# Kernel optimization log

Hardware: AMD Instinct MI355X
Metric: run time of the kernel (lower is better)

The kernel has to match this reference:

```python
import jax, jax.numpy as jnp
import numpy as np

NEG_SLOPE = 0.2


def _gat_conv(x, src, dst, W, a_l, a_r, b, n_nodes, activate):
    """DGL-style GATConv. x:[N,F_in], W:[F_in,H*D], a_l/a_r/b:[H,D]."""
    H, D = a_l.shape
    feat = (x @ W).reshape(n_nodes, H, D)                      # [N,H,D]
    el = jnp.sum(feat * a_l, axis=-1)                          # [N,H]
    er = jnp.sum(feat * a_r, axis=-1)                          # [N,H]
    e = jax.nn.leaky_relu(el[src] + er[dst], NEG_SLOPE)        # [E,H]
    # edge softmax over incoming edges of each dst node (numerically stable)
    emax = jax.ops.segment_max(e, dst, num_segments=n_nodes)   # [N,H]
    emax = jnp.where(jnp.isfinite(emax), emax, 0.0)            # zero-in-degree safe
    ee = jnp.exp(e - emax[dst])                                # [E,H]
    denom = jax.ops.segment_sum(ee, dst, num_segments=n_nodes) # [N,H]
    alpha = ee / jnp.maximum(denom[dst], 1e-9)                 # [E,H]
    # aggregate alpha-weighted src features into dst
    msg = alpha[:, :, None] * feat[src]                        # [E,H,D]
    out = jax.ops.segment_sum(msg, dst, num_segments=n_nodes)  # [N,H,D]
    out = out + b
    if activate:
        out = jax.nn.elu(out)
    return out


def setup_inputs() -> dict:
    key = jax.random.key(0)
    ks = jax.random.split(key, 16)
    N, E, F_in, H, Dh, C = 50000, 800000, 256, 4, 64, 40
    s = lambda fan_in: 1.0 / np.sqrt(fan_in)
    return {
        "x": jax.random.normal(ks[0], (N, F_in), dtype=jnp.float32),
        "edge_index": jax.random.randint(ks[1], (2, E), 0, N, dtype=jnp.int32),
        "W0": jax.random.normal(ks[2], (F_in, H * Dh), dtype=jnp.float32) * s(F_in),
        "al0": jax.random.normal(ks[3], (H, Dh), dtype=jnp.float32) * s(Dh),
        "ar0": jax.random.normal(ks[4], (H, Dh), dtype=jnp.float32) * s(Dh),
        "b0": jnp.zeros((H, Dh), dtype=jnp.float32),
        "W1": jax.random.normal(ks[5], (H * Dh, H * Dh), dtype=jnp.float32) * s(H * Dh),
        "al1": jax.random.normal(ks[6], (H, Dh), dtype=jnp.float32) * s(Dh),
        "ar1": jax.random.normal(ks[7], (H, Dh), dtype=jnp.float32) * s(Dh),
        "b1": jnp.zeros((H, Dh), dtype=jnp.float32),
        "W2": jax.random.normal(ks[8], (H * Dh, H * C), dtype=jnp.float32) * s(H * Dh),
        "al2": jax.random.normal(ks[9], (H, C), dtype=jnp.float32) * s(C),
        "ar2": jax.random.normal(ks[10], (H, C), dtype=jnp.float32) * s(C),
        "b2": jnp.zeros((H, C), dtype=jnp.float32),
    }


def reference(x, edge_index, W0, al0, ar0, b0, W1, al1, ar1, b1, W2, al2, ar2, b2):
    N = x.shape[0]
    src, dst = edge_index[0], edge_index[1]
    h = _gat_conv(x, src, dst, W0, al0, ar0, b0, N, activate=True).reshape(N, -1)
    h = _gat_conv(h, src, dst, W1, al1, ar1, b1, N, activate=True).reshape(N, -1)
    out = _gat_conv(h, src, dst, W2, al2, ar2, b2, N, activate=False)
    logits = out.mean(axis=1)  # mean over heads -> [N, num_classes]
    return logits
```

## Files before the change

kernel.cpp:

```cpp
#include <hip/hip_runtime.h>
#include <hip/hip_bf16.h>
#include <math.h>

#define NEG_SLOPE 0.2f

typedef unsigned short ushortT;
typedef __attribute__((ext_vector_type(8))) short short8;
typedef __attribute__((ext_vector_type(4))) float f32x4;

static __device__ __forceinline__ float leaky(float x){ return x > 0.f ? x : NEG_SLOPE * x; }
static __device__ __forceinline__ float elu(float x){ return x > 0.f ? x : (__expf(x) - 1.f); }

static __device__ __forceinline__ ushortT f2bf(float f){
  unsigned u = __float_as_uint(f);
  u += 0x7fff + ((u >> 16) & 1);
  return (ushortT)(u >> 16);
}
static __device__ __forceinline__ float bf2f(ushortT h){ return __uint_as_float((unsigned)h << 16); }
static __device__ __forceinline__ float bf_lo(unsigned u){ return __uint_as_float(u << 16); }
static __device__ __forceinline__ float bf_hi(unsigned u){ return __uint_as_float(u & 0xffff0000u); }


__global__ void hist_kernel(const int* __restrict__ dst, int E, int* __restrict__ counts){
  int i = blockIdx.x*blockDim.x + threadIdx.x;
  if(i < E) atomicAdd(&counts[dst[i]], 1);
}

__global__ void scan1_kernel(const int* __restrict__ counts, int N,
                             int* __restrict__ offsets, int* __restrict__ blocksums){
  __shared__ int sdata[1024];
  int i = blockIdx.x*1024 + threadIdx.x;
  int v = (i<N) ? counts[i] : 0;
  sdata[threadIdx.x] = v;
  __syncthreads();
  for(int off=1; off<1024; off<<=1){
    int t = (threadIdx.x >= off) ? sdata[threadIdx.x-off] : 0;
    __syncthreads();
    sdata[threadIdx.x] += t;
    __syncthreads();
  }
  if(i<N) offsets[i] = sdata[threadIdx.x] - v;
  if(threadIdx.x==1023) blocksums[blockIdx.x] = sdata[1023];
}

__global__ void scan2_kernel(int* __restrict__ blocksums, int nb){
  __shared__ int sdata[64];
  int v = ((int)threadIdx.x < nb) ? blocksums[threadIdx.x] : 0;
  sdata[threadIdx.x] = v;
  __syncthreads();
  for(int off=1; off<64; off<<=1){
    int t = (threadIdx.x >= off) ? sdata[threadIdx.x-off] : 0;
    __syncthreads();
    sdata[threadIdx.x] += t;
    __syncthreads();
  }
  if((int)threadIdx.x < nb) blocksums[threadIdx.x] = sdata[threadIdx.x] - v;
}

__global__ void scan3_kernel(int* __restrict__ offsets, const int* __restrict__ blocksums,
                             int N, int E, int* __restrict__ cursor){
  int i = blockIdx.x*1024 + threadIdx.x;
  if(i < N){
    int o = offsets[i] + blocksums[blockIdx.x];
    offsets[i] = o;
    cursor[i] = o;
  }
  if(i == 0) offsets[N] = E;
}

__global__ void scatter_kernel(const int* __restrict__ src, const int* __restrict__ dst, int E,
                               int* __restrict__ cursor, int* __restrict__ ssrc,
                               int* __restrict__ sdst){
  int i = blockIdx.x*blockDim.x + threadIdx.x;
  if(i < E){
    int d = dst[i];
    int p = atomicAdd(&cursor[d], 1);
    ssrc[p] = src[i];
    sdst[p] = d;
  }
}

__global__ __launch_bounds__(256) void wsplit_pack(const float* __restrict__ W, int N,
                              ushortT* __restrict__ Wh, ushortT* __restrict__ Wl){
  int idx = blockIdx.x*256 + threadIdx.x;
  int lane = idx & 63;
  int t  = (idx >> 6) & 7;
  int nt = idx >> 9;
  int l15 = lane & 15, quad = lane >> 4;
  int n = nt*16 + l15;
  ushortT h[8], l[8];
  #pragma unroll
  for(int j=0;j<8;j++){
    int k = t*32 + quad*8 + j;
    float v = (n < N) ? W[(size_t)k*N + n] : 0.f;
    h[j] = f2bf(v);
    l[j] = f2bf(v - bf2f(h[j]));
  }
  *(short8*)&Wh[(size_t)idx*8] = *(short8*)h;
  *(short8*)&Wl[(size_t)idx*8] = *(short8*)l;
}

__global__ __launch_bounds__(256) void xsplit_pack(const float* __restrict__ x, int M, int Mpad,
                              ushortT* __restrict__ Xh, ushortT* __restrict__ Xl){
  int idx = blockIdx.x*256 + threadIdx.x;
  if(idx >= 8*Mpad) return;
  int t = idx / Mpad, m = idx - t*Mpad;
  size_t base = (size_t)idx * 32;
  if(m < M){
    const float* xr = &x[(size_t)m*256 + t*32];
    #pragma unroll
    for(int c=0;c<4;c++){
      float4 v0 = *(const float4*)&xr[c*8];
      float4 v1 = *(const float4*)&xr[c*8+4];
      float vv[8] = {v0.x,v0.y,v0.z,v0.w,v1.x,v1.y,v1.z,v1.w};
      ushortT h[8], l[8];
      #pragma unroll
      for(int j=0;j<8;j++){
        h[j] = f2bf(vv[j]);
        l[j] = f2bf(vv[j] - bf2f(h[j]));
      }
      *(short8*)&Xh[base + c*8] = *(short8*)h;
      *(short8*)&Xl[base + c*8] = *(short8*)l;
    }
  } else {
    short8 z = {0,0,0,0,0,0,0,0};
    #pragma unroll
    for(int c=0;c<4;c++){ *(short8*)&Xh[base + c*8] = z; *(short8*)&Xl[base + c*8] = z; }
  }
}

__global__ __launch_bounds__(256) void gemm_packed(
    const ushortT* __restrict__ Ah, const ushortT* __restrict__ Al,
    const ushortT* __restrict__ Bh, const ushortT* __restrict__ Bl,
    ushortT* __restrict__ Cm, int M, int Mpad, int N,
    const float* __restrict__ al, const float* __restrict__ ar,
    float* __restrict__ el, float* __restrict__ er){
  const int lane = threadIdx.x & 63;
  const int wv   = threadIdx.x >> 6;
  const int l15  = lane & 15, quad = lane >> 4;
  const int m0   = blockIdx.x*32;
  const int n0   = wv*64;
  const int nt0  = n0 >> 4;

  f32x4 acc[2][4];
  #pragma unroll
  for(int i=0;i<2;i++)
    #pragma unroll
    for(int j=0;j<4;j++){ acc[i][j][0]=0.f; acc[i][j][1]=0.f; acc[i][j][2]=0.f; acc[i][j][3]=0.f; }

  #pragma unroll
  for(int t=0; t<8; t++){
    short8 a_h[2], a_l[2], b_h[4], b_l[4];
    #pragma unroll
    for(int i=0;i<2;i++){
      size_t ad = ((size_t)t*Mpad + (m0 + i*16 + l15))*32 + quad*8;
      a_h[i] = *(const short8*)&Ah[ad];
      a_l[i] = *(const short8*)&Al[ad];
    }
    #pragma unroll
    for(int j=0;j<4;j++){
      size_t bd = (((size_t)(nt0+j)*8 + t)*64 + lane)*8;
      b_h[j] = *(const short8*)&Bh[bd];
      b_l[j] = *(const short8*)&Bl[bd];
    }
    #pragma unroll
    for(int i=0;i<2;i++)
      #pragma unroll
      for(int j=0;j<4;j++){
        acc[i][j] = __builtin_amdgcn_mfma_f32_16x16x32_bf16(a_h[i], b_h[j], acc[i][j], 0,0,0);
        acc[i][j] = __builtin_amdgcn_mfma_f32_16x16x32_bf16(a_h[i], b_l[j], acc[i][j], 0,0,0);
        acc[i][j] = __builtin_amdgcn_mfma_f32_16x16x32_bf16(a_l[i], b_h[j], acc[i][j], 0,0,0);
      }
  }

  if(al){
    const int h = wv;
    float alv[4], arv[4];
    #pragma unroll
    for(int j=0;j<4;j++){
      alv[j] = al[h*64 + j*16 + l15];
      arv[j] = ar[h*64 + j*16 + l15];
    }
    #pragma unroll
    for(int i=0;i<2;i++){
      #pragma unroll
      for(int r=0;r<4;r++){
        float pl = acc[i][0][r]*alv[0] + acc[i][1][r]*alv[1]
                 + acc[i][2][r]*alv[2] + acc[i][3][r]*alv[3];
        float pr = acc[i][0][r]*arv[0] + acc[i][1][r]*arv[1]
                 + acc[i][2][r]*arv[2] + acc[i][3][r]*arv[3];
        #pragma unroll
        for(int off=1; off<16; off<<=1){ pl += __shfl_xor(pl,off); pr += __shfl_xor(pr,off); }
        int gm = m0 + i*16 + quad*4 + r;
        if(l15==0 && gm < M){ el[gm*4+h] = pl; er[gm*4+h] = pr; }
      }
    }
  }

  #pragma unroll
  for(int i=0;i<2;i++){
    #pragma unroll
    for(int r=0;r<4;r++){
      int gm = m0 + i*16 + quad*4 + r;
      if(gm >= M) continue;
      #pragma unroll
      for(int j=0;j<4;j++){
        int gn = n0 + j*16 + l15;
        if(gn < N) Cm[(size_t)gm*N + gn] = f2bf(acc[i][j][r]);
      }
    }
  }
}

__global__ void attn_proj_bf(const __hip_bfloat16* __restrict__ feat, const float* __restrict__ a_l,
                             const float* __restrict__ a_r, float* __restrict__ el,
                             float* __restrict__ er, int D){
  int n = blockIdx.x;
  int h = threadIdx.x >> 6;
  int lane = threadIdx.x & 63;
  float vl = 0.f, vr = 0.f;
  for(int d=lane; d<D; d+=64){
    float f = (float)feat[(size_t)n*4*D + h*D + d];
    vl = fmaf(f, a_l[h*D+d], vl);
    vr = fmaf(f, a_r[h*D+d], vr);
  }
  #pragma unroll
  for(int off=32; off; off>>=1){ vl += __shfl_down(vl,off); vr += __shfl_down(vr,off); }
  if(lane==0){ el[n*4+h] = vl; er[n*4+h] = vr; }
}

__global__ __launch_bounds__(256) void edge_w_kernel(const int* __restrict__ ssrc,
                              const int* __restrict__ sdst, int E,
                              const float4* __restrict__ el4, const float4* __restrict__ er4,
                              float4* __restrict__ ew){
  int e = blockIdx.x*blockDim.x + threadIdx.x;
  if(e >= E) return;
  int s = ssrc[e], d = sdst[e];
  float4 l = el4[s], r = er4[d];
  float4 w;
  w.x = __expf(leaky(l.x + r.x));
  w.y = __expf(leaky(l.y + r.y));
  w.z = __expf(leaky(l.z + r.z));
  w.w = __expf(leaky(l.w + r.w));
  ew[e] = w;
}

__global__ __launch_bounds__(256) void agg_kernel(const uint2* __restrict__ feat2,
                           const float* __restrict__ ew,
                           const int* __restrict__ offsets, const int* __restrict__ ssrc,
                           const float* __restrict__ bias,
                           ushortT* __restrict__ Hh, ushortT* __restrict__ Hl, int N, int Mpad){
  int wv = threadIdx.x >> 6;
  int lane = threadIdx.x & 63;
  int n = blockIdx.x*4 + wv;
  if(n >= N) return;
  int h = lane >> 4;
  int e0 = offsets[n], e1 = offsets[n+1];
  float4 acc0 = make_float4(0.f,0.f,0.f,0.f), acc1 = acc0, acc2 = acc0, acc3 = acc0;
  float den0 = 0.f, den1 = 0.f, den2 = 0.f, den3 = 0.f;
  int e = e0;
  for(; e+3 < e1; e += 4){
    int s0 = ssrc[e], s1 = ssrc[e+1], s2 = ssrc[e+2], s3 = ssrc[e+3];
    float w0 = ew[(size_t)e*4 + h];
    float w1 = ew[(size_t)(e+1)*4 + h];
    float w2 = ew[(size_t)(e+2)*4 + h];
    float w3 = ew[(size_t)(e+3)*4 + h];
    uint2 q0 = feat2[(size_t)s0*64 + lane];
    uint2 q1 = feat2[(size_t)s1*64 + lane];
    uint2 q2 = feat2[(size_t)s2*64 + lane];
    uint2 q3 = feat2[(size_t)s3*64 + lane];
    acc0.x = fmaf(w0,bf_lo(q0.x),acc0.x); acc0.y = fmaf(w0,bf_hi(q0.x),acc0.y);
    acc0.z = fmaf(w0,bf_lo(q0.y),acc0.z); acc0.w = fmaf(w0,bf_hi(q0.y),acc0.w); den0 += w0;
    acc1.x = fmaf(w1,bf_lo(q1.x),acc1.x); acc1.y = fmaf(w1,bf_hi(q1.x),acc1.y);
    acc1.z = fmaf(w1,bf_lo(q1.y),acc1.z); acc1.w = fmaf(w1,bf_hi(q1.y),acc1.w); den1 += w1;
    acc2.x = fmaf(w2,bf_lo(q2.x),acc2.x); acc2.y = fmaf(w2,bf_hi(q2.x),acc2.y);
    acc2.z = fmaf(w2,bf_lo(q2.y),acc2.z); acc2.w = fmaf(w2,bf_hi(q2.y),acc2.w); den2 += w2;
    acc3.x = fmaf(w3,bf_lo(q3.x),acc3.x); acc3.y = fmaf(w3,bf_hi(q3.x),acc3.y);
    acc3.z = fmaf(w3,bf_lo(q3.y),acc3.z); acc3.w = fmaf(w3,bf_hi(q3.y),acc3.w); den3 += w3;
  }
  for(; e < e1; e++){
    int s = ssrc[e];
    float w = ew[(size_t)e*4 + h];
    uint2 q = feat2[(size_t)s*64 + lane];
    acc0.x = fmaf(w,bf_lo(q.x),acc0.x); acc0.y = fmaf(w,bf_hi(q.x),acc0.y);
    acc0.z = fmaf(w,bf_lo(q.y),acc0.z); acc0.w = fmaf(w,bf_hi(q.y),acc0.w); den0 += w;
  }
  float denom = (den0+den1) + (den2+den3);
  float4 acc;
  acc.x = (acc0.x+acc1.x) + (acc2.x+acc3.x);
  acc.y = (acc0.y+acc1.y) + (acc2.y+acc3.y);
  acc.z = (acc0.z+acc1.z) + (acc2.z+acc3.z);
  acc.w = (acc0.w+acc1.w) + (acc2.w+acc3.w);
  float inv = 1.f / fmaxf(denom, 1e-9f);
  float4 b4 = *(const float4*)&bias[lane*4];
  float o0 = elu(acc.x*inv + b4.x);
  float o1 = elu(acc.y*inv + b4.y);
  float o2 = elu(acc.z*inv + b4.z);
  float o3 = elu(acc.w*inv + b4.w);
  ushortT h0=f2bf(o0), h1=f2bf(o1), h2=f2bf(o2), h3=f2bf(o3);
  ushort4 hv = make_ushort4(h0,h1,h2,h3);
  ushort4 lv = make_ushort4(f2bf(o0-bf2f(h0)), f2bf(o1-bf2f(h1)),
                            f2bf(o2-bf2f(h2)), f2bf(o3-bf2f(h3)));
  int t8 = lane >> 3;
  int co = (lane & 7) * 4;
  size_t ad = ((size_t)t8*Mpad + n)*32 + co;
  *(ushort4*)&Hh[ad] = hv;
  *(ushort4*)&Hl[ad] = lv;
}

__global__ __launch_bounds__(256) void agg2_kernel(const uint2* __restrict__ feat2,
                            const float* __restrict__ ew,
                            const int* __restrict__ offsets, const int* __restrict__ ssrc,
                            const float* __restrict__ bias, float* __restrict__ logits, int N){
  __shared__ float s_out[4][160];
  int wv = threadIdx.x >> 6;
  int lane = threadIdx.x & 63;
  int n = blockIdx.x*4 + wv;
  bool valid = (n < N);
  if(valid && lane < 40){
    int h = lane / 10;
    int e0 = offsets[n], e1 = offsets[n+1];
    float4 acc0 = make_float4(0.f,0.f,0.f,0.f), acc1 = acc0, acc2 = acc0, acc3 = acc0;
    float den0 = 0.f, den1 = 0.f, den2 = 0.f, den3 = 0.f;
    int e = e0;
    for(; e+3 < e1; e += 4){
      int s0 = ssrc[e], s1 = ssrc[e+1], s2 = ssrc[e+2], s3 = ssrc[e+3];
      float w0 = ew[(size_t)e*4 + h];
      float w1 = ew[(size_t)(e+1)*4 + h];
      float w2 = ew[(size_t)(e+2)*4 + h];
      float w3 = ew[(size_t)(e+3)*4 + h];
      uint2 q0 = feat2[(size_t)s0*40 + lane];
      uint2 q1 = feat2[(size_t)s1*40 + lane];
      uint2 q2 = feat2[(size_t)s2*40 + lane];
      uint2 q3 = feat2[(size_t)s3*40 + lane];
      acc0.x = fmaf(w0,bf_lo(q0.x),acc0.x); acc0.y = fmaf(w0,bf_hi(q0.x),acc0.y);
      acc0.z = fmaf(w0,bf_lo(q0.y),acc0.z); acc0.w = fmaf(w0,bf_hi(q0.y),acc0.w); den0 += w0;
      acc1.x = fmaf(w1,bf_lo(q1.x),acc1.x); acc1.y = fmaf(w1,bf_hi(q1.x),acc1.y);
      acc1.z = fmaf(w1,bf_lo(q1.y),acc1.z); acc1.w = fmaf(w1,bf_hi(q1.y),acc1.w); den1 += w1;
      acc2.x = fmaf(w2,bf_lo(q2.x),acc2.x); acc2.y = fmaf(w2,bf_hi(q2.x),acc2.y);
      acc2.z = fmaf(w2,bf_lo(q2.y),acc2.z); acc2.w = fmaf(w2,bf_hi(q2.y),acc2.w); den2 += w2;
      acc3.x = fmaf(w3,bf_lo(q3.x),acc3.x); acc3.y = fmaf(w3,bf_hi(q3.x),acc3.y);
      acc3.z = fmaf(w3,bf_lo(q3.y),acc3.z); acc3.w = fmaf(w3,bf_hi(q3.y),acc3.w); den3 += w3;
    }
    for(; e < e1; e++){
      int s = ssrc[e];
      float w = ew[(size_t)e*4 + h];
      uint2 q = feat2[(size_t)s*40 + lane];
      acc0.x = fmaf(w,bf_lo(q.x),acc0.x); acc0.y = fmaf(w,bf_hi(q.x),acc0.y);
      acc0.z = fmaf(w,bf_lo(q.y),acc0.z); acc0.w = fmaf(w,bf_hi(q.y),acc0.w); den0 += w;
    }
    float denom = (den0+den1) + (den2+den3);
    float4 acc;
    acc.x = (acc0.x+acc1.x) + (acc2.x+acc3.x);
    acc.y = (acc0.y+acc1.y) + (acc2.y+acc3.y);
    acc.z = (acc0.z+acc1.z) + (acc2.z+acc3.z);
    acc.w = (acc0.w+acc1.w) + (acc2.w+acc3.w);
    float inv = 1.f / fmaxf(denom, 1e-9f);
    float4 b4 = *(const float4*)&bias[lane*4];
    s_out[wv][lane*4+0] = acc.x*inv + b4.x;
    s_out[wv][lane*4+1] = acc.y*inv + b4.y;
    s_out[wv][lane*4+2] = acc.z*inv + b4.z;
    s_out[wv][lane*4+3] = acc.w*inv + b4.w;
  }
  __syncthreads();
  if(valid && lane < 40){
    logits[(size_t)n*40 + lane] =
        0.25f * (s_out[wv][lane] + s_out[wv][40+lane] + s_out[wv][80+lane] + s_out[wv][120+lane]);
  }
}

extern "C" void kernel_launch(void* const* d_in, const int* in_sizes, int n_in,
                              void* d_out, int out_size, void* d_ws, size_t ws_size,
                              hipStream_t stream){
  const float* x   = (const float*)d_in[0];
  const int*   eix = (const int*)  d_in[1];
  const float* W0  = (const float*)d_in[2];
  const float* al0 = (const float*)d_in[3];
  const float* ar0 = (const float*)d_in[4];
  const float* b0  = (const float*)d_in[5];
  const float* W1  = (const float*)d_in[6];
  const float* al1 = (const float*)d_in[7];
  const float* ar1 = (const float*)d_in[8];
  const float* b1  = (const float*)d_in[9];
  const float* W2  = (const float*)d_in[10];
  const float* al2 = (const float*)d_in[11];
  const float* ar2 = (const float*)d_in[12];
  const float* b2  = (const float*)d_in[13];
  float* logits = (float*)d_out;

  const int N = in_sizes[0] / 256;
  const int E = in_sizes[1] / 2;
  const int* src = eix;
  const int* dst = eix + E;
  const int nb = (N + 1023) / 1024;

  char* ws = (char*)d_ws;
  auto alloc = [&](size_t bytes)->char*{
    char* p = ws; ws += (bytes + 255) & ~(size_t)255; return p;
  };
  const int nblocksM = (N + 127)/128;
  const int Mpad = nblocksM * 128;
  const size_t apackElems = (size_t)Mpad * 256;
  int*   counts    = (int*)  alloc((size_t)N*4);
  int*   offsets   = (int*)  alloc((size_t)(N+1)*4);
  int*   cursor    = (int*)  alloc((size_t)N*4);
  int*   blocksums = (int*)  alloc((size_t)nb*4);
  int*   ssrc      = (int*)  alloc((size_t)E*4);
  int*   sdst      = (int*)  alloc((size_t)E*4);
  float* ew        = (float*)alloc((size_t)E*4*4);
  __hip_bfloat16* bufF = (__hip_bfloat16*)alloc((size_t)N*256*2);
  ushortT* Hh      = (ushortT*)alloc(apackElems*2);
  ushortT* Hl      = (ushortT*)alloc(apackElems*2);
  float* el_buf    = (float*)alloc((size_t)N*4*4);
  float* er_buf    = (float*)alloc((size_t)N*4*4);
  ushortT* Wph0 = (ushortT*)alloc(16*8*64*8*2);
  ushortT* Wpl0 = (ushortT*)alloc(16*8*64*8*2);
  ushortT* Wph1 = (ushortT*)alloc(16*8*64*8*2);
  ushortT* Wpl1 = (ushortT*)alloc(16*8*64*8*2);
  ushortT* Wph2 = (ushortT*)alloc(16*8*64*8*2);
  ushortT* Wpl2 = (ushortT*)alloc(16*8*64*8*2);

  hipMemsetAsync(counts, 0, (size_t)N*4, stream);
  hist_kernel   <<<(E+255)/256, 256, 0, stream>>>(dst, E, counts);
  scan1_kernel  <<<nb, 1024, 0, stream>>>(counts, N, offsets, blocksums);
  scan2_kernel  <<<1, 64, 0, stream>>>(blocksums, nb);
  scan3_kernel  <<<nb, 1024, 0, stream>>>(offsets, blocksums, N, E, cursor);
  scatter_kernel<<<(E+255)/256, 256, 0, stream>>>(src, dst, E, cursor, ssrc, sdst);

  wsplit_pack<<<32, 256, 0, stream>>>(W0, 256, Wph0, Wpl0);
  wsplit_pack<<<32, 256, 0, stream>>>(W1, 256, Wph1, Wpl1);
  wsplit_pack<<<32, 256, 0, stream>>>(W2, 160, Wph2, Wpl2);
  int xtotal = 8 * Mpad;
  xsplit_pack<<<(xtotal+255)/256, 256, 0, stream>>>(x, N, Mpad, Hh, Hl);

  int ggBlocks = Mpad / 32;
  int aggGrid = (N+3)/4;
  int ewGrid  = (E+255)/256;
  gemm_packed<<<ggBlocks, 256, 0, stream>>>(Hh, Hl, Wph0, Wpl0, (ushortT*)bufF, N, Mpad, 256, al0, ar0, el_buf, er_buf);
  edge_w_kernel<<<ewGrid, 256, 0, stream>>>(ssrc, sdst, E, (const float4*)el_buf, (const float4*)er_buf, (float4*)ew);
  agg_kernel<<<aggGrid, 256, 0, stream>>>((const uint2*)bufF, ew, offsets, ssrc, b0, Hh, Hl, N, Mpad);
  gemm_packed<<<ggBlocks, 256, 0, stream>>>(Hh, Hl, Wph1, Wpl1, (ushortT*)bufF, N, Mpad, 256, al1, ar1, el_buf, er_buf);
  edge_w_kernel<<<ewGrid, 256, 0, stream>>>(ssrc, sdst, E, (const float4*)el_buf, (const float4*)er_buf, (float4*)ew);
  agg_kernel<<<aggGrid, 256, 0, stream>>>((const uint2*)bufF, ew, offsets, ssrc, b1, Hh, Hl, N, Mpad);
  gemm_packed<<<ggBlocks, 256, 0, stream>>>(Hh, Hl, Wph2, Wpl2, (ushortT*)bufF, N, Mpad, 160, nullptr, nullptr, nullptr, nullptr);
  attn_proj_bf<<<N, 256, 0, stream>>>(bufF, al2, ar2, el_buf, er_buf, 40);
  edge_w_kernel<<<ewGrid, 256, 0, stream>>>(ssrc, sdst, E, (const float4*)el_buf, (const float4*)er_buf, (float4*)ew);
  agg2_kernel<<<aggGrid, 256, 0, stream>>>((const uint2*)bufF, ew, offsets, ssrc, b2, logits, N);
}
```

Before: 561.3 us.

## Split aggregation into per-column-chunk blocks with head-major edge weights

Edge weights are now stored head-major (four planes of E floats) instead of interleaved float4, and the layer-0/1 aggregation is split into 8 column chunks per node. Within a wave, 8 edge groups each gather one 8-byte slice per lane and are reduced with xor shuffles. Loads and stores use nontemporal hints. The goal is more parallelism and better gather locality per block (32-column slices), at the cost of 8x more blocks, repeated reads of offsets and ssrc for each chunk, and a shuffle reduction.

```diff
diff --git a/kernel.cpp b/kernel.cpp
--- a/kernel.cpp
+++ b/kernel.cpp
@@ -232,86 +232,77 @@
 __global__ __launch_bounds__(256) void edge_w_kernel(const int* __restrict__ ssrc,
                               const int* __restrict__ sdst, int E,
                               const float4* __restrict__ el4, const float4* __restrict__ er4,
-                              float4* __restrict__ ew){
+                              float* __restrict__ ewp){
   int e = blockIdx.x*blockDim.x + threadIdx.x;
   if(e >= E) return;
   int s = ssrc[e], d = sdst[e];
   float4 l = el4[s], r = er4[d];
-  float4 w;
-  w.x = __expf(leaky(l.x + r.x));
-  w.y = __expf(leaky(l.y + r.y));
-  w.z = __expf(leaky(l.z + r.z));
-  w.w = __expf(leaky(l.w + r.w));
-  ew[e] = w;
-}
-
-__global__ __launch_bounds__(256) void agg_kernel(const uint2* __restrict__ feat2,
-                           const float* __restrict__ ew,
+  ewp[e]              = __expf(leaky(l.x + r.x));
+  ewp[(size_t)E + e]  = __expf(leaky(l.y + r.y));
+  ewp[(size_t)2*E + e]= __expf(leaky(l.z + r.z));
+  ewp[(size_t)3*E + e]= __expf(leaky(l.w + r.w));
+}
+
+__global__ __launch_bounds__(256) void agg_chunk_kernel(const uint2* __restrict__ feat2,
+                           const float* __restrict__ ewp,
                            const int* __restrict__ offsets, const int* __restrict__ ssrc,
                            const float* __restrict__ bias,
-                           ushortT* __restrict__ Hh, ushortT* __restrict__ Hl, int N, int Mpad){
-  int wv = threadIdx.x >> 6;
-  int lane = threadIdx.x & 63;
-  int n = blockIdx.x*4 + wv;
+                           ushortT* __restrict__ Hh, ushortT* __restrict__ Hl,
+                           int N, int Mpad, int E){
+  const int c   = blockIdx.x & 7;
+  const int nb  = blockIdx.x >> 3;
+  const int wv  = threadIdx.x >> 6;
+  const int lane= threadIdx.x & 63;
+  const int n = nb*4 + wv;
   if(n >= N) return;
-  int h = lane >> 4;
+  const int dl = lane & 7;
+  const int eg = lane >> 3;
+  const float* __restrict__ wh = ewp + (size_t)(c >> 1) * E;
+  const uint2* __restrict__ fc = feat2 + c*8 + dl;
   int e0 = offsets[n], e1 = offsets[n+1];
-  float4 acc0 = make_float4(0.f,0.f,0.f,0.f), acc1 = acc0, acc2 = acc0, acc3 = acc0;
-  float den0 = 0.f, den1 = 0.f, den2 = 0.f, den3 = 0.f;
-  int e = e0;
-  for(; e+3 < e1; e += 4){
-    int s0 = ssrc[e], s1 = ssrc[e+1], s2 = ssrc[e+2], s3 = ssrc[e+3];
-    float w0 = ew[(size_t)e*4 + h];
-    float w1 = ew[(size_t)(e+1)*4 + h];
-    float w2 = ew[(size_t)(e+2)*4 + h];
-    float w3 = ew[(size_t)(e+3)*4 + h];
-    uint2 q0 = feat2[(size_t)s0*64 + lane];
-    uint2 q1 = feat2[(size_t)s1*64 + lane];
-    uint2 q2 = feat2[(size_t)s2*64 + lane];
-    uint2 q3 = feat2[(size_t)s3*64 + lane];
-    acc0.x = fmaf(w0,bf_lo(q0.x),acc0.x); acc0.y = fmaf(w0,bf_hi(q0.x),acc0.y);
-    acc0.z = fmaf(w0,bf_lo(q0.y),acc0.z); acc0.w = fmaf(w0,bf_hi(q0.y),acc0.w); den0 += w0;
-    acc1.x = fmaf(w1,bf_lo(q1.x),acc1.x); acc1.y = fmaf(w1,bf_hi(q1.x),acc1.y);
-    acc1.z = fmaf(w1,bf_lo(q1.y),acc1.z); acc1.w = fmaf(w1,bf_hi(q1.y),acc1.w); den1 += w1;
-    acc2.x = fmaf(w2,bf_lo(q2.x),acc2.x); acc2.y = fmaf(w2,bf_hi(q2.x),acc2.y);
-    acc2.z = fmaf(w2,bf_lo(q2.y),acc2.z); acc2.w = fmaf(w2,bf_hi(q2.y),acc2.w); den2 += w2;
-    acc3.x = fmaf(w3,bf_lo(q3.x),acc3.x); acc3.y = fmaf(w3,bf_hi(q3.x),acc3.y);
-    acc3.z = fmaf(w3,bf_lo(q3.y),acc3.z); acc3.w = fmaf(w3,bf_hi(q3.y),acc3.w); den3 += w3;
-  }
-  for(; e < e1; e++){
-    int s = ssrc[e];
-    float w = ew[(size_t)e*4 + h];
-    uint2 q = feat2[(size_t)s*64 + lane];
-    acc0.x = fmaf(w,bf_lo(q.x),acc0.x); acc0.y = fmaf(w,bf_hi(q.x),acc0.y);
-    acc0.z = fmaf(w,bf_lo(q.y),acc0.z); acc0.w = fmaf(w,bf_hi(q.y),acc0.w); den0 += w;
-  }
-  float denom = (den0+den1) + (den2+den3);
-  float4 acc;
-  acc.x = (acc0.x+acc1.x) + (acc2.x+acc3.x);
-  acc.y = (acc0.y+acc1.y) + (acc2.y+acc3.y);
-  acc.z = (acc0.z+acc1.z) + (acc2.z+acc3.z);
-  acc.w = (acc0.w+acc1.w) + (acc2.w+acc3.w);
-  float inv = 1.f / fmaxf(denom, 1e-9f);
-  float4 b4 = *(const float4*)&bias[lane*4];
-  float o0 = elu(acc.x*inv + b4.x);
-  float o1 = elu(acc.y*inv + b4.y);
-  float o2 = elu(acc.z*inv + b4.z);
-  float o3 = elu(acc.w*inv + b4.w);
-  ushortT h0=f2bf(o0), h1=f2bf(o1), h2=f2bf(o2), h3=f2bf(o3);
-  ushort4 hv = make_ushort4(h0,h1,h2,h3);
-  ushort4 lv = make_ushort4(f2bf(o0-bf2f(h0)), f2bf(o1-bf2f(h1)),
-                            f2bf(o2-bf2f(h2)), f2bf(o3-bf2f(h3)));
-  int t8 = lane >> 3;
-  int co = (lane & 7) * 4;
-  size_t ad = ((size_t)t8*Mpad + n)*32 + co;
-  *(ushort4*)&Hh[ad] = hv;
-  *(ushort4*)&Hl[ad] = lv;
+  float4 acc = make_float4(0.f,0.f,0.f,0.f);
+  float den = 0.f;
+  for(int e = e0 + eg; e < e1; e += 8){
+    int s   = __builtin_nontemporal_load(&ssrc[e]);
+    float w = __builtin_nontemporal_load(&wh[e]);
+    uint2 q = fc[(size_t)s*64];
+    acc.x = fmaf(w, bf_lo(q.x), acc.x);
+    acc.y = fmaf(w, bf_hi(q.x), acc.y);
+    acc.z = fmaf(w, bf_lo(q.y), acc.z);
+    acc.w = fmaf(w, bf_hi(q.y), acc.w);
+    den += w;
+  }
+  #pragma unroll
+  for(int off=8; off<64; off<<=1){
+    acc.x += __shfl_xor(acc.x, off);
+    acc.y += __shfl_xor(acc.y, off);
+    acc.z += __shfl_xor(acc.z, off);
+    acc.w += __shfl_xor(acc.w, off);
+    den   += __shfl_xor(den, off);
+  }
+  if(eg == 0){
+    float inv = 1.f / fmaxf(den, 1e-9f);
+    int k = c*32 + dl*4;
+    float4 b4 = *(const float4*)&bias[k];
+    float o0 = elu(acc.x*inv + b4.x);
+    float o1 = elu(acc.y*inv + b4.y);
+    float o2 = elu(acc.z*inv + b4.z);
+    float o3 = elu(acc.w*inv + b4.w);
+    ushortT h0=f2bf(o0), h1=f2bf(o1), h2=f2bf(o2), h3=f2bf(o3);
+    ushort4 hv = make_ushort4(h0,h1,h2,h3);
+    ushort4 lv = make_ushort4(f2bf(o0-bf2f(h0)), f2bf(o1-bf2f(h1)),
+                              f2bf(o2-bf2f(h2)), f2bf(o3-bf2f(h3)));
+    size_t ad = ((size_t)c*Mpad + n)*32 + (size_t)dl*4;
+    __builtin_nontemporal_store(*(unsigned long long*)&hv, (unsigned long long*)&Hh[ad]);
+    __builtin_nontemporal_store(*(unsigned long long*)&lv, (unsigned long long*)&Hl[ad]);
+  }
 }
 
 __global__ __launch_bounds__(256) void agg2_kernel(const uint2* __restrict__ feat2,
-                            const float* __restrict__ ew,
+                            const float* __restrict__ ewp,
                             const int* __restrict__ offsets, const int* __restrict__ ssrc,
-                            const float* __restrict__ bias, float* __restrict__ logits, int N){
+                            const float* __restrict__ bias, float* __restrict__ logits,
+                            int N, int E){
   __shared__ float s_out[4][160];
   int wv = threadIdx.x >> 6;
   int lane = threadIdx.x & 63;
@@ -319,16 +310,17 @@
   bool valid = (n < N);
   if(valid && lane < 40){
     int h = lane / 10;
+    const float* __restrict__ wh = ewp + (size_t)h * E;
     int e0 = offsets[n], e1 = offsets[n+1];
     float4 acc0 = make_float4(0.f,0.f,0.f,0.f), acc1 = acc0, acc2 = acc0, acc3 = acc0;
     float den0 = 0.f, den1 = 0.f, den2 = 0.f, den3 = 0.f;
     int e = e0;
     for(; e+3 < e1; e += 4){
       int s0 = ssrc[e], s1 = ssrc[e+1], s2 = ssrc[e+2], s3 = ssrc[e+3];
-      float w0 = ew[(size_t)e*4 + h];
-      float w1 = ew[(size_t)(e+1)*4 + h];
-      float w2 = ew[(size_t)(e+2)*4 + h];
-      float w3 = ew[(size_t)(e+3)*4 + h];
+      float w0 = wh[e];
+      float w1 = wh[e+1];
+      float w2 = wh[e+2];
+      float w3 = wh[e+3];
       uint2 q0 = feat2[(size_t)s0*40 + lane];
       uint2 q1 = feat2[(size_t)s1*40 + lane];
       uint2 q2 = feat2[(size_t)s2*40 + lane];
@@ -344,7 +336,7 @@
     }
     for(; e < e1; e++){
       int s = ssrc[e];
-      float w = ew[(size_t)e*4 + h];
+      float w = wh[e];
       uint2 q = feat2[(size_t)s*40 + lane];
       acc0.x = fmaf(w,bf_lo(q.x),acc0.x); acc0.y = fmaf(w,bf_hi(q.x),acc0.y);
       acc0.z = fmaf(w,bf_lo(q.y),acc0.z); acc0.w = fmaf(w,bf_hi(q.y),acc0.w); den0 += w;
@@ -434,16 +426,17 @@
   xsplit_pack<<<(xtotal+255)/256, 256, 0, stream>>>(x, N, Mpad, Hh, Hl);
 
   int ggBlocks = Mpad / 32;
-  int aggGrid = (N+3)/4;
+  int aggGrid  = (N+3)/4;
+  int aggChunkGrid = 8 * aggGrid;
   int ewGrid  = (E+255)/256;
   gemm_packed<<<ggBlocks, 256, 0, stream>>>(Hh, Hl, Wph0, Wpl0, (ushortT*)bufF, N, Mpad, 256, al0, ar0, el_buf, er_buf);
-  edge_w_kernel<<<ewGrid, 256, 0, stream>>>(ssrc, sdst, E, (const float4*)el_buf, (const float4*)er_buf, (float4*)ew);
-  agg_kernel<<<aggGrid, 256, 0, stream>>>((const uint2*)bufF, ew, offsets, ssrc, b0, Hh, Hl, N, Mpad);
+  edge_w_kernel<<<ewGrid, 256, 0, stream>>>(ssrc, sdst, E, (const float4*)el_buf, (const float4*)er_buf, ew);
+  agg_chunk_kernel<<<aggChunkGrid, 256, 0, stream>>>((const uint2*)bufF, ew, offsets, ssrc, b0, Hh, Hl, N, Mpad, E);
   gemm_packed<<<ggBlocks, 256, 0, stream>>>(Hh, Hl, Wph1, Wpl1, (ushortT*)bufF, N, Mpad, 256, al1, ar1, el_buf, er_buf);
-  edge_w_kernel<<<ewGrid, 256, 0, stream>>>(ssrc, sdst, E, (const float4*)el_buf, (const float4*)er_buf, (float4*)ew);
-  agg_kernel<<<aggGrid, 256, 0, stream>>>((const uint2*)bufF, ew, offsets, ssrc, b1, Hh, Hl, N, Mpad);
+  edge_w_kernel<<<ewGrid, 256, 0, stream>>>(ssrc, sdst, E, (const float4*)el_buf, (const float4*)er_buf, ew);
+  agg_chunk_kernel<<<aggChunkGrid, 256, 0, stream>>>((const uint2*)bufF, ew, offsets, ssrc, b1, Hh, Hl, N, Mpad, E);
   gemm_packed<<<ggBlocks, 256, 0, stream>>>(Hh, Hl, Wph2, Wpl2, (ushortT*)bufF, N, Mpad, 160, nullptr, nullptr, nullptr, nullptr);
   attn_proj_bf<<<N, 256, 0, stream>>>(bufF, al2, ar2, el_buf, er_buf, 40);
-  edge_w_kernel<<<ewGrid, 256, 0, stream>>>(ssrc, sdst, E, (const float4*)el_buf, (const float4*)er_buf, (float4*)ew);
-  agg2_kernel<<<aggGrid, 256, 0, stream>>>((const uint2*)bufF, ew, offsets, ssrc, b2, logits, N);
-}
+  edge_w_kernel<<<ewGrid, 256, 0, stream>>>(ssrc, sdst, E, (const float4*)el_buf, (const float4*)er_buf, ew);
+  agg2_kernel<<<aggGrid, 256, 0, stream>>>((const uint2*)bufF, ew, offsets, ssrc, b2, logits, N, E);
+}
```

Result: slower. 897.3 us (+59.9%).
